# Kernel optimization log

Measured on AMD Instinct MI355X. Metric: run time of the kernel, lower is better.

Reference implementation:

```python
import jax, jax.numpy as jnp
import numpy as np
import math

D_KEY = 64
SCALE = math.sqrt(D_KEY)
INF = 1e10  # finite stand-in for the original INF constant
CAUSAL = True
DIAG = False


def setup_inputs() -> dict:
    key = jax.random.key(0)
    kq, kk, kv = jax.random.split(key, 3)
    B, L, D = 16, 2048, D_KEY
    return {
        "query": jax.random.normal(kq, (B, L, D), dtype=jnp.float32),
        "key": jax.random.normal(kk, (B, L, D), dtype=jnp.float32),
        "value": jax.random.normal(kv, (B, L, D), dtype=jnp.float32),
    }


def reference(query, key, value):
    # scores: [B, Lq, Lk]
    scores = jnp.einsum("bqd,bkd->bqk", query, key)
    L = key.shape[1]
    if CAUSAL:
        # subtract INF above the diagonal (strict upper triangle), as in torch triu(1)
        tri = jnp.triu(jnp.full((L, L), INF, dtype=scores.dtype), k=1)
        scores = scores - tri[None, :, :]
    if DIAG:
        # original scatters -INF onto the diagonal along dim 1
        diag_mask = jnp.eye(L, dtype=bool)
        scores = jnp.where(diag_mask[None, :, :], -INF, scores)
    # softmax over keys after scaling; dropout with p=0.0 is identity
    attn = jax.nn.softmax(scores / SCALE, axis=-1)
    return jnp.einsum("bqk,bkd->bqd", attn, value)
```

## Files before the change

kernel.cpp:

```cpp
#include <hip/hip_runtime.h>

typedef __bf16 bf16_t;
typedef __bf16 bf16x4 __attribute__((ext_vector_type(4)));
typedef __bf16 bf16x8 __attribute__((ext_vector_type(8)));
typedef float  f32x4  __attribute__((ext_vector_type(4)));

#define B_SZ  16
#define L_SEQ 2048
#define D_H   64
#define QB    64
#define KB    128
#define NQT   (L_SEQ / QB)

#define QSCALE 0.18033688011112043f

__global__ __launch_bounds__(256, 2)
void attn_fwd_kernel(const float* __restrict__ Qg, const float* __restrict__ Kg,
                     const float* __restrict__ Vg, float* __restrict__ Og)
{
    const int lin  = blockIdx.x;
    const int xcd  = lin & 7;
    const int slot = lin >> 3;
    const int half = slot >> 5;
    const int qi   = slot & 31;
    const int b    = xcd * 2 + half;
    const int qt   = half ? qi : (31 - qi);

    const int tid  = threadIdx.x;
    const int lane = tid & 63;
    const int lg   = lane >> 4;
    const int lc   = lane & 15;

    __shared__ __align__(16) bf16_t K_lds[2][KB][72];
    __shared__ __align__(16) bf16_t Vt_lds[2][D_H][136];

    const size_t bbase = (size_t)b * L_SEQ * D_H;

    const int qrow = qt * QB + (tid >> 6) * 16 + lc;
    bf16x8 qa[2];
#pragma unroll
    for (int h = 0; h < 2; ++h) {
        const float* qp = Qg + bbase + (size_t)qrow * D_H + h * 32 + lg * 8;
        const f32x4 f0 = *reinterpret_cast<const f32x4*>(qp);
        const f32x4 f1 = *reinterpret_cast<const f32x4*>(qp + 4);
        bf16x8 a;
#pragma unroll
        for (int j = 0; j < 4; ++j) { a[j] = (bf16_t)(f0[j] * QSCALE); a[4 + j] = (bf16_t)(f1[j] * QSCALE); }
        qa[h] = a;
    }

    f32x4 o[4];
#pragma unroll
    for (int dt = 0; dt < 4; ++dt) o[dt] = (f32x4){0.f, 0.f, 0.f, 0.f};
    float m = -1e30f, l = 0.f;

    const int nkt = (qt + 2) >> 1;

    const int vkb = tid & 31;
    const int vdg = tid >> 5;
    const int vpos = ((vkb >> 3) << 5) + ((vkb & 3) << 3) + (((vkb >> 2) & 1) << 2);

    f32x4 kreg[8], vreg[8];

    auto issueK = [&](int kt) {
        const int kbase = kt * KB;
#pragma unroll
        for (int i = 0; i < 8; ++i) {
            const int f = i * 256 + tid;
            const int r = f >> 4, c4 = (f & 15) * 4;
            kreg[i] = *reinterpret_cast<const f32x4*>(Kg + bbase + (size_t)(kbase + r) * D_H + c4);
        }
    };
    auto issueV = [&](int kt) {
        const int kbase = kt * KB;
#pragma unroll
        for (int d2 = 0; d2 < 2; ++d2)
#pragma unroll
            for (int i = 0; i < 4; ++i)
                vreg[d2 * 4 + i] = *reinterpret_cast<const f32x4*>(
                    Vg + bbase + (size_t)(kbase + vkb * 4 + i) * D_H + (vdg + d2 * 8) * 4);
    };
    auto writeK = [&](int buf) {
#pragma unroll
        for (int i = 0; i < 8; ++i) {
            const int f = i * 256 + tid;
            const int r = f >> 4, c4 = (f & 15) * 4;
            bf16x4 k4 = { (bf16_t)kreg[i][0], (bf16_t)kreg[i][1], (bf16_t)kreg[i][2], (bf16_t)kreg[i][3] };
            *reinterpret_cast<bf16x4*>(&K_lds[buf][r][c4]) = k4;
        }
    };
    auto writeV = [&](int buf) {
#pragma unroll
        for (int d2 = 0; d2 < 2; ++d2) {
            const int db = vdg + d2 * 8;
#pragma unroll
            for (int j = 0; j < 4; ++j) {
                bf16x4 cj = { (bf16_t)vreg[d2 * 4 + 0][j], (bf16_t)vreg[d2 * 4 + 1][j],
                              (bf16_t)vreg[d2 * 4 + 2][j], (bf16_t)vreg[d2 * 4 + 3][j] };
                *reinterpret_cast<bf16x4*>(&Vt_lds[buf][db * 4 + j][vpos]) = cj;
            }
        }
    };

    issueK(0); issueV(0); writeK(0); writeV(0);
    __syncthreads();
    int cur = 0;
    for (int kt = 0; kt < nkt; ++kt) {
        const bool last = (kt == nkt - 1);
        const int kbase = kt * KB;
        if (!last) issueK(kt + 1);

        f32x4 s[8];
        __builtin_amdgcn_s_setprio(1);
#pragma unroll
        for (int n = 0; n < 8; ++n) {
            f32x4 acc = (f32x4){0.f, 0.f, 0.f, 0.f};
#pragma unroll
            for (int h = 0; h < 2; ++h) {
                const bf16x8 kb = *reinterpret_cast<const bf16x8*>(&K_lds[cur][n * 16 + lc][h * 32 + lg * 8]);
                acc = __builtin_amdgcn_mfma_f32_16x16x32_bf16(kb, qa[h], acc, 0, 0, 0);
            }
            s[n] = acc;
        }
        __builtin_amdgcn_s_setprio(0);
        if (!last) issueV(kt + 1);
        if (last) {
#pragma unroll
            for (int n = 0; n < 8; ++n)
#pragma unroll
                for (int r = 0; r < 4; ++r)
                    if (kbase + n * 16 + lg * 4 + r > qrow) s[n][r] = -1e30f;
        }

        float mx = -1e30f;
#pragma unroll
        for (int n = 0; n < 8; ++n) {
            mx = fmaxf(fmaxf(mx, s[n][0]), fmaxf(s[n][1], fmaxf(s[n][2], s[n][3])));
        }
        mx = fmaxf(mx, __shfl_xor(mx, 16));
        mx = fmaxf(mx, __shfl_xor(mx, 32));
        const float mn = fmaxf(m, mx);
        const float alpha = exp2f(m - mn);
        m = mn;
        bf16x8 w[4];
        float rs = 0.f;
#pragma unroll
        for (int n = 0; n < 8; ++n) {
            const float p0 = exp2f(s[n][0] - mn), p1 = exp2f(s[n][1] - mn);
            const float p2 = exp2f(s[n][2] - mn), p3 = exp2f(s[n][3] - mn);
            rs += (p0 + p1) + (p2 + p3);
            const int wi = n >> 1, off = (n & 1) * 4;
            w[wi][off + 0] = (bf16_t)p0; w[wi][off + 1] = (bf16_t)p1;
            w[wi][off + 2] = (bf16_t)p2; w[wi][off + 3] = (bf16_t)p3;
        }
        rs += __shfl_xor(rs, 16);
        rs += __shfl_xor(rs, 32);
        l = l * alpha + rs;
#pragma unroll
        for (int dt = 0; dt < 4; ++dt)
#pragma unroll
            for (int r = 0; r < 4; ++r) o[dt][r] *= alpha;

        if (!last) writeK(cur ^ 1);

        __builtin_amdgcn_s_setprio(1);
#pragma unroll
        for (int ks = 0; ks < 4; ++ks) {
#pragma unroll
            for (int dt = 0; dt < 4; ++dt) {
                const bf16x8 vb = *reinterpret_cast<const bf16x8*>(&Vt_lds[cur][dt * 16 + lc][ks * 32 + lg * 8]);
                o[dt] = __builtin_amdgcn_mfma_f32_16x16x32_bf16(vb, w[ks], o[dt], 0, 0, 0);
            }
        }
        __builtin_amdgcn_s_setprio(0);

        if (!last) writeV(cur ^ 1);
        __syncthreads();
        cur ^= 1;
    }

    const float inv = 1.0f / l;
#pragma unroll
    for (int dt = 0; dt < 4; ++dt) {
        f32x4 val = { o[dt][0] * inv, o[dt][1] * inv, o[dt][2] * inv, o[dt][3] * inv };
        *reinterpret_cast<f32x4*>(Og + bbase + (size_t)qrow * D_H + dt * 16 + lg * 4) = val;
    }
}

extern "C" void kernel_launch(void* const* d_in, const int* in_sizes, int n_in,
                              void* d_out, int out_size, void* d_ws, size_t ws_size,
                              hipStream_t stream)
{
    const float* Q = (const float*)d_in[0];
    const float* K = (const float*)d_in[1];
    const float* V = (const float*)d_in[2];
    float* O = (float*)d_out;
    attn_fwd_kernel<<<dim3(NQT * B_SZ), dim3(256), 0, stream>>>(Q, K, V, O);
}
```

Before: 39.70 us.

## Split KV range across two wave groups and pair complementary causal q-tiles per block

Blocks grow to 512 threads, organised as two 256-thread groups. The groups process alternating KV tiles for the same query tile, and their partial softmax states (m, l, O) are merged through LDS at the end. Each block handles a pair of complementary query tiles (qt and 31-qt) in sequence, which balances causal work per block, and the grid shrinks to 256 blocks. This aims to improve load balance and per-tile parallelism. In exchange it doubles LDS use, adds merge synchronisation, and leaves fewer blocks to hide latency.

```diff
diff --git a/kernel.cpp b/kernel.cpp
--- a/kernel.cpp
+++ b/kernel.cpp
@@ -10,54 +10,33 @@
 #define D_H   64
 #define QB    64
 #define KB    128
-#define NQT   (L_SEQ / QB)
 
 #define QSCALE 0.18033688011112043f
 
-__global__ __launch_bounds__(256, 2)
+__global__ __launch_bounds__(512, 2)
 void attn_fwd_kernel(const float* __restrict__ Qg, const float* __restrict__ Kg,
                      const float* __restrict__ Vg, float* __restrict__ Og)
 {
-    const int lin  = blockIdx.x;
-    const int xcd  = lin & 7;
-    const int slot = lin >> 3;
-    const int half = slot >> 5;
-    const int qi   = slot & 31;
-    const int b    = xcd * 2 + half;
-    const int qt   = half ? qi : (31 - qi);
+    const int lin = blockIdx.x;
+    const int xcd = lin & 7;
+    const int b   = xcd * 2 + ((lin >> 3) & 1);
+    const int pi  = lin >> 4;
 
     const int tid  = threadIdx.x;
+    const int grp  = tid >> 8;
+    const int t8   = tid & 255;
+    const int wig  = t8 >> 6;
     const int lane = tid & 63;
     const int lg   = lane >> 4;
     const int lc   = lane & 15;
 
-    __shared__ __align__(16) bf16_t K_lds[2][KB][72];
-    __shared__ __align__(16) bf16_t Vt_lds[2][D_H][136];
+    __shared__ __align__(16) bf16_t K_lds[2][2][KB][72];
+    __shared__ __align__(16) bf16_t Vt_lds[2][2][D_H][136];
 
     const size_t bbase = (size_t)b * L_SEQ * D_H;
 
-    const int qrow = qt * QB + (tid >> 6) * 16 + lc;
-    bf16x8 qa[2];
-#pragma unroll
-    for (int h = 0; h < 2; ++h) {
-        const float* qp = Qg + bbase + (size_t)qrow * D_H + h * 32 + lg * 8;
-        const f32x4 f0 = *reinterpret_cast<const f32x4*>(qp);
-        const f32x4 f1 = *reinterpret_cast<const f32x4*>(qp + 4);
-        bf16x8 a;
-#pragma unroll
-        for (int j = 0; j < 4; ++j) { a[j] = (bf16_t)(f0[j] * QSCALE); a[4 + j] = (bf16_t)(f1[j] * QSCALE); }
-        qa[h] = a;
-    }
-
-    f32x4 o[4];
-#pragma unroll
-    for (int dt = 0; dt < 4; ++dt) o[dt] = (f32x4){0.f, 0.f, 0.f, 0.f};
-    float m = -1e30f, l = 0.f;
-
-    const int nkt = (qt + 2) >> 1;
-
-    const int vkb = tid & 31;
-    const int vdg = tid >> 5;
+    const int vkb  = t8 & 31;
+    const int vdg  = t8 >> 5;
     const int vpos = ((vkb >> 3) << 5) + ((vkb & 3) << 3) + (((vkb >> 2) & 1) << 2);
 
     f32x4 kreg[8], vreg[8];
@@ -66,7 +45,7 @@
         const int kbase = kt * KB;
 #pragma unroll
         for (int i = 0; i < 8; ++i) {
-            const int f = i * 256 + tid;
+            const int f = i * 256 + t8;
             const int r = f >> 4, c4 = (f & 15) * 4;
             kreg[i] = *reinterpret_cast<const f32x4*>(Kg + bbase + (size_t)(kbase + r) * D_H + c4);
         }
@@ -83,10 +62,10 @@
     auto writeK = [&](int buf) {
 #pragma unroll
         for (int i = 0; i < 8; ++i) {
-            const int f = i * 256 + tid;
+            const int f = i * 256 + t8;
             const int r = f >> 4, c4 = (f & 15) * 4;
             bf16x4 k4 = { (bf16_t)kreg[i][0], (bf16_t)kreg[i][1], (bf16_t)kreg[i][2], (bf16_t)kreg[i][3] };
-            *reinterpret_cast<bf16x4*>(&K_lds[buf][r][c4]) = k4;
+            *reinterpret_cast<bf16x4*>(&K_lds[grp][buf][r][c4]) = k4;
         }
     };
     auto writeV = [&](int buf) {
@@ -97,93 +76,142 @@
             for (int j = 0; j < 4; ++j) {
                 bf16x4 cj = { (bf16_t)vreg[d2 * 4 + 0][j], (bf16_t)vreg[d2 * 4 + 1][j],
                               (bf16_t)vreg[d2 * 4 + 2][j], (bf16_t)vreg[d2 * 4 + 3][j] };
-                *reinterpret_cast<bf16x4*>(&Vt_lds[buf][db * 4 + j][vpos]) = cj;
+                *reinterpret_cast<bf16x4*>(&Vt_lds[grp][buf][db * 4 + j][vpos]) = cj;
             }
         }
     };
 
-    issueK(0); issueV(0); writeK(0); writeV(0);
-    __syncthreads();
-    int cur = 0;
-    for (int kt = 0; kt < nkt; ++kt) {
-        const bool last = (kt == nkt - 1);
-        const int kbase = kt * KB;
-        if (!last) issueK(kt + 1);
-
-        f32x4 s[8];
-        __builtin_amdgcn_s_setprio(1);
-#pragma unroll
-        for (int n = 0; n < 8; ++n) {
-            f32x4 acc = (f32x4){0.f, 0.f, 0.f, 0.f};
-#pragma unroll
-            for (int h = 0; h < 2; ++h) {
-                const bf16x8 kb = *reinterpret_cast<const bf16x8*>(&K_lds[cur][n * 16 + lc][h * 32 + lg * 8]);
-                acc = __builtin_amdgcn_mfma_f32_16x16x32_bf16(kb, qa[h], acc, 0, 0, 0);
+    for (int hv = 0; hv < 2; ++hv) {
+        const int qt  = hv ? pi : (31 - pi);
+        const int nkt = (qt + 2) >> 1;
+        const int nsG = (nkt + 1 - grp) >> 1;
+        const int ns0 = (nkt + 1) >> 1;
+
+        const int qrow = qt * QB + wig * 16 + lc;
+        bf16x8 qa[2];
+#pragma unroll
+        for (int h = 0; h < 2; ++h) {
+            const float* qp = Qg + bbase + (size_t)qrow * D_H + h * 32 + lg * 8;
+            const f32x4 f0 = *reinterpret_cast<const f32x4*>(qp);
+            const f32x4 f1 = *reinterpret_cast<const f32x4*>(qp + 4);
+            bf16x8 a;
+#pragma unroll
+            for (int j = 0; j < 4; ++j) { a[j] = (bf16_t)(f0[j] * QSCALE); a[4 + j] = (bf16_t)(f1[j] * QSCALE); }
+            qa[h] = a;
+        }
+
+        f32x4 o[4];
+#pragma unroll
+        for (int dt = 0; dt < 4; ++dt) o[dt] = (f32x4){0.f, 0.f, 0.f, 0.f};
+        float m = -1e30f, l = 0.f;
+
+        if (nsG > 0) { issueK(grp); issueV(grp); writeK(0); writeV(0); }
+        __syncthreads();
+
+        int cur = 0;
+        for (int s = 0; s < ns0; ++s) {
+            if (s < nsG) {
+                const int kt    = 2 * s + grp;
+                const int kbase = kt * KB;
+                const bool more = (s + 1 < nsG);
+                if (more) issueK(2 * (s + 1) + grp);
+
+                f32x4 sc[8];
+                __builtin_amdgcn_s_setprio(1);
+#pragma unroll
+                for (int n = 0; n < 8; ++n) {
+                    f32x4 acc = (f32x4){0.f, 0.f, 0.f, 0.f};
+#pragma unroll
+                    for (int h = 0; h < 2; ++h) {
+                        const bf16x8 kb = *reinterpret_cast<const bf16x8*>(&K_lds[grp][cur][n * 16 + lc][h * 32 + lg * 8]);
+                        acc = __builtin_amdgcn_mfma_f32_16x16x32_bf16(kb, qa[h], acc, 0, 0, 0);
+                    }
+                    sc[n] = acc;
+                }
+                __builtin_amdgcn_s_setprio(0);
+                if (more) issueV(2 * (s + 1) + grp);
+                if (kt == nkt - 1) {
+#pragma unroll
+                    for (int n = 0; n < 8; ++n)
+#pragma unroll
+                        for (int r = 0; r < 4; ++r)
+                            if (kbase + n * 16 + lg * 4 + r > qrow) sc[n][r] = -1e30f;
+                }
+
+                float mx = -1e30f;
+#pragma unroll
+                for (int n = 0; n < 8; ++n)
+                    mx = fmaxf(fmaxf(mx, sc[n][0]), fmaxf(sc[n][1], fmaxf(sc[n][2], sc[n][3])));
+                mx = fmaxf(mx, __shfl_xor(mx, 16));
+                mx = fmaxf(mx, __shfl_xor(mx, 32));
+                const float mn = fmaxf(m, mx);
+                const float alpha = exp2f(m - mn);
+                m = mn;
+                bf16x8 w[4];
+                float rs = 0.f;
+#pragma unroll
+                for (int n = 0; n < 8; ++n) {
+                    const float p0 = exp2f(sc[n][0] - mn), p1 = exp2f(sc[n][1] - mn);
+                    const float p2 = exp2f(sc[n][2] - mn), p3 = exp2f(sc[n][3] - mn);
+                    rs += (p0 + p1) + (p2 + p3);
+                    const int wi = n >> 1, off = (n & 1) * 4;
+                    w[wi][off + 0] = (bf16_t)p0; w[wi][off + 1] = (bf16_t)p1;
+                    w[wi][off + 2] = (bf16_t)p2; w[wi][off + 3] = (bf16_t)p3;
+                }
+                rs += __shfl_xor(rs, 16);
+                rs += __shfl_xor(rs, 32);
+                l = l * alpha + rs;
+#pragma unroll
+                for (int dt = 0; dt < 4; ++dt)
+#pragma unroll
+                    for (int r = 0; r < 4; ++r) o[dt][r] *= alpha;
+
+                if (more) writeK(cur ^ 1);
+
+                __builtin_amdgcn_s_setprio(1);
+#pragma unroll
+                for (int ks = 0; ks < 4; ++ks) {
+#pragma unroll
+                    for (int dt = 0; dt < 4; ++dt) {
+                        const bf16x8 vb = *reinterpret_cast<const bf16x8*>(&Vt_lds[grp][cur][dt * 16 + lc][ks * 32 + lg * 8]);
+                        o[dt] = __builtin_amdgcn_mfma_f32_16x16x32_bf16(vb, w[ks], o[dt], 0, 0, 0);
+                    }
+                }
+                __builtin_amdgcn_s_setprio(0);
+
+                if (more) writeV(cur ^ 1);
             }
-            s[n] = acc;
-        }
-        __builtin_amdgcn_s_setprio(0);
-        if (!last) issueV(kt + 1);
-        if (last) {
-#pragma unroll
-            for (int n = 0; n < 8; ++n)
-#pragma unroll
-                for (int r = 0; r < 4; ++r)
-                    if (kbase + n * 16 + lg * 4 + r > qrow) s[n][r] = -1e30f;
-        }
-
-        float mx = -1e30f;
-#pragma unroll
-        for (int n = 0; n < 8; ++n) {
-            mx = fmaxf(fmaxf(mx, s[n][0]), fmaxf(s[n][1], fmaxf(s[n][2], s[n][3])));
-        }
-        mx = fmaxf(mx, __shfl_xor(mx, 16));
-        mx = fmaxf(mx, __shfl_xor(mx, 32));
-        const float mn = fmaxf(m, mx);
-        const float alpha = exp2f(m - mn);
-        m = mn;
-        bf16x8 w[4];
-        float rs = 0.f;
-#pragma unroll
-        for (int n = 0; n < 8; ++n) {
-            const float p0 = exp2f(s[n][0] - mn), p1 = exp2f(s[n][1] - mn);
-            const float p2 = exp2f(s[n][2] - mn), p3 = exp2f(s[n][3] - mn);
-            rs += (p0 + p1) + (p2 + p3);
-            const int wi = n >> 1, off = (n & 1) * 4;
-            w[wi][off + 0] = (bf16_t)p0; w[wi][off + 1] = (bf16_t)p1;
-            w[wi][off + 2] = (bf16_t)p2; w[wi][off + 3] = (bf16_t)p3;
-        }
-        rs += __shfl_xor(rs, 16);
-        rs += __shfl_xor(rs, 32);
-        l = l * alpha + rs;
-#pragma unroll
-        for (int dt = 0; dt < 4; ++dt)
-#pragma unroll
-            for (int r = 0; r < 4; ++r) o[dt][r] *= alpha;
-
-        if (!last) writeK(cur ^ 1);
-
-        __builtin_amdgcn_s_setprio(1);
-#pragma unroll
-        for (int ks = 0; ks < 4; ++ks) {
+            __syncthreads();
+            cur ^= 1;
+        }
+
+        float* mrg  = reinterpret_cast<float*>(&K_lds[0][0][0][0]);
+        float* obuf = mrg;
+        float* mbuf = mrg + 64 * 68;
+        float* lbuf = mrg + 64 * 68 + 64;
+        const int qq = wig * 16 + lc;
+        if (grp == 1) {
+#pragma unroll
+            for (int dt = 0; dt < 4; ++dt)
+                *reinterpret_cast<f32x4*>(&obuf[qq * 68 + dt * 16 + lg * 4]) = o[dt];
+            if (lg == 0) { mbuf[qq] = m; lbuf[qq] = l; }
+        }
+        __syncthreads();
+        if (grp == 0) {
+            const float m1 = mbuf[qq], l1 = lbuf[qq];
+            const float mt = fmaxf(m, m1);
+            const float a0 = exp2f(m - mt), a1 = exp2f(m1 - mt);
+            const float linv = 1.0f / (l * a0 + l1 * a1);
 #pragma unroll
             for (int dt = 0; dt < 4; ++dt) {
-                const bf16x8 vb = *reinterpret_cast<const bf16x8*>(&Vt_lds[cur][dt * 16 + lc][ks * 32 + lg * 8]);
-                o[dt] = __builtin_amdgcn_mfma_f32_16x16x32_bf16(vb, w[ks], o[dt], 0, 0, 0);
+                const f32x4 o1 = *reinterpret_cast<const f32x4*>(&obuf[qq * 68 + dt * 16 + lg * 4]);
+                f32x4 val;
+#pragma unroll
+                for (int r = 0; r < 4; ++r) val[r] = (o[dt][r] * a0 + o1[r] * a1) * linv;
+                *reinterpret_cast<f32x4*>(Og + bbase + (size_t)qrow * D_H + dt * 16 + lg * 4) = val;
             }
         }
-        __builtin_amdgcn_s_setprio(0);
-
-        if (!last) writeV(cur ^ 1);
         __syncthreads();
-        cur ^= 1;
-    }
-
-    const float inv = 1.0f / l;
-#pragma unroll
-    for (int dt = 0; dt < 4; ++dt) {
-        f32x4 val = { o[dt][0] * inv, o[dt][1] * inv, o[dt][2] * inv, o[dt][3] * inv };
-        *reinterpret_cast<f32x4*>(Og + bbase + (size_t)qrow * D_H + dt * 16 + lg * 4) = val;
     }
 }
 
@@ -195,5 +223,5 @@
     const float* K = (const float*)d_in[1];
     const float* V = (const float*)d_in[2];
     float* O = (float*)d_out;
-    attn_fwd_kernel<<<dim3(NQT * B_SZ), dim3(256), 0, stream>>>(Q, K, V, O);
+    attn_fwd_kernel<<<dim3(256), dim3(512), 0, stream>>>(Q, K, V, O);
 }
```

New measurement: 40.36 us. Within noise of the previous version (+1.7%).

## Swizzle K/V shared-memory layout, lazily rescale softmax, defer row-sum reduction

Applied to the files above, without the earlier changes.

Replaces the padded K and transposed-V LDS arrays with unpadded XOR-swizzled layouts and widens the K global loads and LDS writes to 8-element chunks. The online softmax now rescales the running max, sum and output only when some lane's new maximum exceeds the old one by more than a threshold of 8 (log2 domain), which skips the exp and multiply work in most iterations. The per-lane row sum is reduced across lanes once at the end instead of every tile. The target is fewer LDS bank conflicts, fewer LDS write instructions and less softmax and shuffle work per tile, at the cost of more index arithmetic and a bound on exponent growth before rescaling.

```diff
diff --git a/kernel.cpp b/kernel.cpp
--- a/kernel.cpp
+++ b/kernel.cpp
@@ -10,7 +10,6 @@
 #define D_H   64
 #define QB    64
 #define KB    128
-#define NQT   (L_SEQ / QB)
 
 #define QSCALE 0.18033688011112043f
 
@@ -30,9 +29,10 @@
     const int lane = tid & 63;
     const int lg   = lane >> 4;
     const int lc   = lane & 15;
-
-    __shared__ __align__(16) bf16_t K_lds[2][KB][72];
-    __shared__ __align__(16) bf16_t Vt_lds[2][D_H][136];
+    const int lc7  = lc & 7;
+
+    __shared__ __align__(16) bf16_t K_lds[2][KB * D_H];
+    __shared__ __align__(16) bf16_t Vt_lds[2][D_H * KB];
 
     const size_t bbase = (size_t)b * L_SEQ * D_H;
 
@@ -56,8 +56,8 @@
 
     const int nkt = (qt + 2) >> 1;
 
-    const int vkb = tid & 31;
-    const int vdg = tid >> 5;
+    const int vkb  = tid & 31;
+    const int vdg  = tid >> 5;
     const int vpos = ((vkb >> 3) << 5) + ((vkb & 3) << 3) + (((vkb >> 2) & 1) << 2);
 
     f32x4 kreg[8], vreg[8];
@@ -65,10 +65,12 @@
     auto issueK = [&](int kt) {
         const int kbase = kt * KB;
 #pragma unroll
-        for (int i = 0; i < 8; ++i) {
-            const int f = i * 256 + tid;
-            const int r = f >> 4, c4 = (f & 15) * 4;
-            kreg[i] = *reinterpret_cast<const f32x4*>(Kg + bbase + (size_t)(kbase + r) * D_H + c4);
+        for (int i = 0; i < 4; ++i) {
+            const int u = i * 256 + tid;
+            const int r = u >> 3, ch = u & 7;
+            const float* p = Kg + bbase + (size_t)(kbase + r) * D_H + ch * 8;
+            kreg[2 * i]     = *reinterpret_cast<const f32x4*>(p);
+            kreg[2 * i + 1] = *reinterpret_cast<const f32x4*>(p + 4);
         }
     };
     auto issueV = [&](int kt) {
@@ -82,11 +84,13 @@
     };
     auto writeK = [&](int buf) {
 #pragma unroll
-        for (int i = 0; i < 8; ++i) {
-            const int f = i * 256 + tid;
-            const int r = f >> 4, c4 = (f & 15) * 4;
-            bf16x4 k4 = { (bf16_t)kreg[i][0], (bf16_t)kreg[i][1], (bf16_t)kreg[i][2], (bf16_t)kreg[i][3] };
-            *reinterpret_cast<bf16x4*>(&K_lds[buf][r][c4]) = k4;
+        for (int i = 0; i < 4; ++i) {
+            const int u = i * 256 + tid;
+            const int r = u >> 3, ch = u & 7;
+            bf16x8 kk;
+#pragma unroll
+            for (int j = 0; j < 4; ++j) { kk[j] = (bf16_t)kreg[2 * i][j]; kk[4 + j] = (bf16_t)kreg[2 * i + 1][j]; }
+            *reinterpret_cast<bf16x8*>(&K_lds[buf][r * 64 + ((ch ^ (r & 7)) << 3)]) = kk;
         }
     };
     auto writeV = [&](int buf) {
@@ -95,9 +99,11 @@
             const int db = vdg + d2 * 8;
 #pragma unroll
             for (int j = 0; j < 4; ++j) {
+                const int d = db * 4 + j;
                 bf16x4 cj = { (bf16_t)vreg[d2 * 4 + 0][j], (bf16_t)vreg[d2 * 4 + 1][j],
                               (bf16_t)vreg[d2 * 4 + 2][j], (bf16_t)vreg[d2 * 4 + 3][j] };
-                *reinterpret_cast<bf16x4*>(&Vt_lds[buf][db * 4 + j][vpos]) = cj;
+                const int hw = d * 128 + (((vpos >> 3) ^ (d & 7)) << 3) + (vpos & 7);
+                *reinterpret_cast<bf16x4*>(&Vt_lds[buf][hw]) = cj;
             }
         }
     };
@@ -110,17 +116,18 @@
         const int kbase = kt * KB;
         if (!last) issueK(kt + 1);
 
-        f32x4 s[8];
+        f32x4 sc[8];
         __builtin_amdgcn_s_setprio(1);
 #pragma unroll
         for (int n = 0; n < 8; ++n) {
             f32x4 acc = (f32x4){0.f, 0.f, 0.f, 0.f};
 #pragma unroll
             for (int h = 0; h < 2; ++h) {
-                const bf16x8 kb = *reinterpret_cast<const bf16x8*>(&K_lds[cur][n * 16 + lc][h * 32 + lg * 8]);
+                const int hw = (n * 16 + lc) * 64 + ((((h << 2) | lg) ^ lc7) << 3);
+                const bf16x8 kb = *reinterpret_cast<const bf16x8*>(&K_lds[cur][hw]);
                 acc = __builtin_amdgcn_mfma_f32_16x16x32_bf16(kb, qa[h], acc, 0, 0, 0);
             }
-            s[n] = acc;
+            sc[n] = acc;
         }
         __builtin_amdgcn_s_setprio(0);
         if (!last) issueV(kt + 1);
@@ -129,37 +136,38 @@
             for (int n = 0; n < 8; ++n)
 #pragma unroll
                 for (int r = 0; r < 4; ++r)
-                    if (kbase + n * 16 + lg * 4 + r > qrow) s[n][r] = -1e30f;
-        }
-
-        float mx = -1e30f;
-#pragma unroll
-        for (int n = 0; n < 8; ++n) {
-            mx = fmaxf(fmaxf(mx, s[n][0]), fmaxf(s[n][1], fmaxf(s[n][2], s[n][3])));
-        }
-        mx = fmaxf(mx, __shfl_xor(mx, 16));
-        mx = fmaxf(mx, __shfl_xor(mx, 32));
-        const float mn = fmaxf(m, mx);
-        const float alpha = exp2f(m - mn);
-        m = mn;
+                    if (kbase + n * 16 + lg * 4 + r > qrow) sc[n][r] = -1e30f;
+        }
+
+        float mxp = fmaxf(fmaxf(sc[0][0], sc[0][1]), fmaxf(sc[0][2], sc[0][3]));
+#pragma unroll
+        for (int n = 1; n < 8; ++n)
+            mxp = fmaxf(mxp, fmaxf(fmaxf(sc[n][0], sc[n][1]), fmaxf(sc[n][2], sc[n][3])));
+        if (!__all(mxp <= m + 8.0f)) {
+            float mx = mxp;
+            mx = fmaxf(mx, __shfl_xor(mx, 16));
+            mx = fmaxf(mx, __shfl_xor(mx, 32));
+            const float mn = fmaxf(m, mx);
+            const float alpha = exp2f(m - mn);
+            m = mn;
+            l *= alpha;
+#pragma unroll
+            for (int dt = 0; dt < 4; ++dt)
+#pragma unroll
+                for (int r = 0; r < 4; ++r) o[dt][r] *= alpha;
+        }
         bf16x8 w[4];
         float rs = 0.f;
 #pragma unroll
         for (int n = 0; n < 8; ++n) {
-            const float p0 = exp2f(s[n][0] - mn), p1 = exp2f(s[n][1] - mn);
-            const float p2 = exp2f(s[n][2] - mn), p3 = exp2f(s[n][3] - mn);
+            const float p0 = exp2f(sc[n][0] - m), p1 = exp2f(sc[n][1] - m);
+            const float p2 = exp2f(sc[n][2] - m), p3 = exp2f(sc[n][3] - m);
             rs += (p0 + p1) + (p2 + p3);
             const int wi = n >> 1, off = (n & 1) * 4;
             w[wi][off + 0] = (bf16_t)p0; w[wi][off + 1] = (bf16_t)p1;
             w[wi][off + 2] = (bf16_t)p2; w[wi][off + 3] = (bf16_t)p3;
         }
-        rs += __shfl_xor(rs, 16);
-        rs += __shfl_xor(rs, 32);
-        l = l * alpha + rs;
-#pragma unroll
-        for (int dt = 0; dt < 4; ++dt)
-#pragma unroll
-            for (int r = 0; r < 4; ++r) o[dt][r] *= alpha;
+        l += rs;
 
         if (!last) writeK(cur ^ 1);
 
@@ -168,7 +176,8 @@
         for (int ks = 0; ks < 4; ++ks) {
 #pragma unroll
             for (int dt = 0; dt < 4; ++dt) {
-                const bf16x8 vb = *reinterpret_cast<const bf16x8*>(&Vt_lds[cur][dt * 16 + lc][ks * 32 + lg * 8]);
+                const int hw = (dt * 16 + lc) * 128 + ((((ks << 2) | lg) ^ lc7) << 3);
+                const bf16x8 vb = *reinterpret_cast<const bf16x8*>(&Vt_lds[cur][hw]);
                 o[dt] = __builtin_amdgcn_mfma_f32_16x16x32_bf16(vb, w[ks], o[dt], 0, 0, 0);
             }
         }
@@ -179,7 +188,10 @@
         cur ^= 1;
     }
 
-    const float inv = 1.0f / l;
+    float lr = l;
+    lr += __shfl_xor(lr, 16);
+    lr += __shfl_xor(lr, 32);
+    const float inv = 1.0f / lr;
 #pragma unroll
     for (int dt = 0; dt < 4; ++dt) {
         f32x4 val = { o[dt][0] * inv, o[dt][1] * inv, o[dt][2] * inv, o[dt][3] * inv };
@@ -195,5 +207,5 @@
     const float* K = (const float*)d_in[1];
     const float* V = (const float*)d_in[2];
     float* O = (float*)d_out;
-    attn_fwd_kernel<<<dim3(NQT * B_SZ), dim3(256), 0, stream>>>(Q, K, V, O);
+    attn_fwd_kernel<<<dim3(512), dim3(256), 0, stream>>>(Q, K, V, O);
 }
```

New measurement: 40.14 us. Within noise of the previous version (+1.1%).

## Split block into producer loader waves and consumer MFMA waves with lazy rescale

Applied to the files above, without the earlier changes.

The block grows to 512 threads. Four waves only load K/V from global memory, convert them to bf16 and write the double-buffered LDS tiles, while the other four waves do the QK and PV MFMAs and the softmax, with the two groups synchronised by block barriers. The consumers also skip the running-max rescale when no lane's new max exceeds the old one by more than a threshold, and defer the cross-lane row-sum reduction to the end. This is meant to overlap global-load latency with compute and to cut softmax ALU and shuffle work. The cost is more threads per CU, possible LDS write/read races around the single barrier per iteration, and some numerical risk from the threshold-based lazy rescale.

```diff
diff --git a/kernel.cpp b/kernel.cpp
--- a/kernel.cpp
+++ b/kernel.cpp
@@ -14,9 +14,9 @@
 
 #define QSCALE 0.18033688011112043f
 
-__global__ __launch_bounds__(256, 2)
-void attn_fwd_kernel(const float* __restrict__ Qg, const float* __restrict__ Kg,
-                     const float* __restrict__ Vg, float* __restrict__ Og)
+__global__ __launch_bounds__(512, 4)
+void attn_pc_kernel(const float* __restrict__ Qg, const float* __restrict__ Kg,
+                    const float* __restrict__ Vg, float* __restrict__ Og)
 {
     const int lin  = blockIdx.x;
     const int xcd  = lin & 7;
@@ -27,6 +27,7 @@
     const int qt   = half ? qi : (31 - qi);
 
     const int tid  = threadIdx.x;
+    const int wave = tid >> 6;
     const int lane = tid & 63;
     const int lg   = lane >> 4;
     const int lc   = lane & 15;
@@ -35,155 +36,164 @@
     __shared__ __align__(16) bf16_t Vt_lds[2][D_H][136];
 
     const size_t bbase = (size_t)b * L_SEQ * D_H;
-
-    const int qrow = qt * QB + (tid >> 6) * 16 + lc;
-    bf16x8 qa[2];
-#pragma unroll
-    for (int h = 0; h < 2; ++h) {
-        const float* qp = Qg + bbase + (size_t)qrow * D_H + h * 32 + lg * 8;
-        const f32x4 f0 = *reinterpret_cast<const f32x4*>(qp);
-        const f32x4 f1 = *reinterpret_cast<const f32x4*>(qp + 4);
-        bf16x8 a;
-#pragma unroll
-        for (int j = 0; j < 4; ++j) { a[j] = (bf16_t)(f0[j] * QSCALE); a[4 + j] = (bf16_t)(f1[j] * QSCALE); }
-        qa[h] = a;
-    }
-
-    f32x4 o[4];
-#pragma unroll
-    for (int dt = 0; dt < 4; ++dt) o[dt] = (f32x4){0.f, 0.f, 0.f, 0.f};
-    float m = -1e30f, l = 0.f;
-
     const int nkt = (qt + 2) >> 1;
 
-    const int vkb = tid & 31;
-    const int vdg = tid >> 5;
-    const int vpos = ((vkb >> 3) << 5) + ((vkb & 3) << 3) + (((vkb >> 2) & 1) << 2);
-
-    f32x4 kreg[8], vreg[8];
-
-    auto issueK = [&](int kt) {
-        const int kbase = kt * KB;
-#pragma unroll
-        for (int i = 0; i < 8; ++i) {
-            const int f = i * 256 + tid;
-            const int r = f >> 4, c4 = (f & 15) * 4;
-            kreg[i] = *reinterpret_cast<const f32x4*>(Kg + bbase + (size_t)(kbase + r) * D_H + c4);
-        }
-    };
-    auto issueV = [&](int kt) {
-        const int kbase = kt * KB;
-#pragma unroll
-        for (int d2 = 0; d2 < 2; ++d2)
-#pragma unroll
-            for (int i = 0; i < 4; ++i)
-                vreg[d2 * 4 + i] = *reinterpret_cast<const f32x4*>(
-                    Vg + bbase + (size_t)(kbase + vkb * 4 + i) * D_H + (vdg + d2 * 8) * 4);
-    };
-    auto writeK = [&](int buf) {
-#pragma unroll
-        for (int i = 0; i < 8; ++i) {
-            const int f = i * 256 + tid;
-            const int r = f >> 4, c4 = (f & 15) * 4;
-            bf16x4 k4 = { (bf16_t)kreg[i][0], (bf16_t)kreg[i][1], (bf16_t)kreg[i][2], (bf16_t)kreg[i][3] };
-            *reinterpret_cast<bf16x4*>(&K_lds[buf][r][c4]) = k4;
-        }
-    };
-    auto writeV = [&](int buf) {
-#pragma unroll
-        for (int d2 = 0; d2 < 2; ++d2) {
-            const int db = vdg + d2 * 8;
-#pragma unroll
-            for (int j = 0; j < 4; ++j) {
-                bf16x4 cj = { (bf16_t)vreg[d2 * 4 + 0][j], (bf16_t)vreg[d2 * 4 + 1][j],
-                              (bf16_t)vreg[d2 * 4 + 2][j], (bf16_t)vreg[d2 * 4 + 3][j] };
-                *reinterpret_cast<bf16x4*>(&Vt_lds[buf][db * 4 + j][vpos]) = cj;
-            }
-        }
-    };
-
-    issueK(0); issueV(0); writeK(0); writeV(0);
-    __syncthreads();
-    int cur = 0;
-    for (int kt = 0; kt < nkt; ++kt) {
-        const bool last = (kt == nkt - 1);
-        const int kbase = kt * KB;
-        if (!last) issueK(kt + 1);
-
-        f32x4 s[8];
-        __builtin_amdgcn_s_setprio(1);
-#pragma unroll
-        for (int n = 0; n < 8; ++n) {
-            f32x4 acc = (f32x4){0.f, 0.f, 0.f, 0.f};
-#pragma unroll
-            for (int h = 0; h < 2; ++h) {
-                const bf16x8 kb = *reinterpret_cast<const bf16x8*>(&K_lds[cur][n * 16 + lc][h * 32 + lg * 8]);
-                acc = __builtin_amdgcn_mfma_f32_16x16x32_bf16(kb, qa[h], acc, 0, 0, 0);
-            }
-            s[n] = acc;
-        }
-        __builtin_amdgcn_s_setprio(0);
-        if (!last) issueV(kt + 1);
-        if (last) {
-#pragma unroll
-            for (int n = 0; n < 8; ++n)
-#pragma unroll
-                for (int r = 0; r < 4; ++r)
-                    if (kbase + n * 16 + lg * 4 + r > qrow) s[n][r] = -1e30f;
-        }
-
-        float mx = -1e30f;
-#pragma unroll
-        for (int n = 0; n < 8; ++n) {
-            mx = fmaxf(fmaxf(mx, s[n][0]), fmaxf(s[n][1], fmaxf(s[n][2], s[n][3])));
-        }
-        mx = fmaxf(mx, __shfl_xor(mx, 16));
-        mx = fmaxf(mx, __shfl_xor(mx, 32));
-        const float mn = fmaxf(m, mx);
-        const float alpha = exp2f(m - mn);
-        m = mn;
-        bf16x8 w[4];
-        float rs = 0.f;
-#pragma unroll
-        for (int n = 0; n < 8; ++n) {
-            const float p0 = exp2f(s[n][0] - mn), p1 = exp2f(s[n][1] - mn);
-            const float p2 = exp2f(s[n][2] - mn), p3 = exp2f(s[n][3] - mn);
-            rs += (p0 + p1) + (p2 + p3);
-            const int wi = n >> 1, off = (n & 1) * 4;
-            w[wi][off + 0] = (bf16_t)p0; w[wi][off + 1] = (bf16_t)p1;
-            w[wi][off + 2] = (bf16_t)p2; w[wi][off + 3] = (bf16_t)p3;
-        }
-        rs += __shfl_xor(rs, 16);
-        rs += __shfl_xor(rs, 32);
-        l = l * alpha + rs;
-#pragma unroll
-        for (int dt = 0; dt < 4; ++dt)
-#pragma unroll
-            for (int r = 0; r < 4; ++r) o[dt][r] *= alpha;
-
-        if (!last) writeK(cur ^ 1);
-
-        __builtin_amdgcn_s_setprio(1);
-#pragma unroll
-        for (int ks = 0; ks < 4; ++ks) {
-#pragma unroll
-            for (int dt = 0; dt < 4; ++dt) {
-                const bf16x8 vb = *reinterpret_cast<const bf16x8*>(&Vt_lds[cur][dt * 16 + lc][ks * 32 + lg * 8]);
-                o[dt] = __builtin_amdgcn_mfma_f32_16x16x32_bf16(vb, w[ks], o[dt], 0, 0, 0);
-            }
-        }
-        __builtin_amdgcn_s_setprio(0);
-
-        if (!last) writeV(cur ^ 1);
+    if (wave >= 4) {
+        const int pt   = tid - 256;
+        const int vkb  = pt & 31;
+        const int vdg  = pt >> 5;
+        const int vpos = ((vkb >> 3) << 5) + ((vkb & 3) << 3) + (((vkb >> 2) & 1) << 2);
+
+        f32x4 kreg[8], vreg[8];
+
+        auto issueK = [&](int kt) {
+            const int kbase = kt * KB;
+#pragma unroll
+            for (int i = 0; i < 8; ++i) {
+                const int f = i * 256 + pt;
+                const int r = f >> 4, c4 = (f & 15) * 4;
+                kreg[i] = *reinterpret_cast<const f32x4*>(Kg + bbase + (size_t)(kbase + r) * D_H + c4);
+            }
+        };
+        auto issueV = [&](int kt) {
+            const int kbase = kt * KB;
+#pragma unroll
+            for (int d2 = 0; d2 < 2; ++d2)
+#pragma unroll
+                for (int i = 0; i < 4; ++i)
+                    vreg[d2 * 4 + i] = *reinterpret_cast<const f32x4*>(
+                        Vg + bbase + (size_t)(kbase + vkb * 4 + i) * D_H + (vdg + d2 * 8) * 4);
+        };
+        auto writeK = [&](int buf) {
+#pragma unroll
+            for (int i = 0; i < 8; ++i) {
+                const int f = i * 256 + pt;
+                const int r = f >> 4, c4 = (f & 15) * 4;
+                bf16x4 k4 = { (bf16_t)kreg[i][0], (bf16_t)kreg[i][1], (bf16_t)kreg[i][2], (bf16_t)kreg[i][3] };
+                *reinterpret_cast<bf16x4*>(&K_lds[buf][r][c4]) = k4;
+            }
+        };
+        auto writeV = [&](int buf) {
+#pragma unroll
+            for (int d2 = 0; d2 < 2; ++d2) {
+                const int db = vdg + d2 * 8;
+#pragma unroll
+                for (int j = 0; j < 4; ++j) {
+                    bf16x4 cj = { (bf16_t)vreg[d2 * 4 + 0][j], (bf16_t)vreg[d2 * 4 + 1][j],
+                                  (bf16_t)vreg[d2 * 4 + 2][j], (bf16_t)vreg[d2 * 4 + 3][j] };
+                    *reinterpret_cast<bf16x4*>(&Vt_lds[buf][db * 4 + j][vpos]) = cj;
+                }
+            }
+        };
+
+        issueK(0); issueV(0); writeK(0); writeV(0);
         __syncthreads();
-        cur ^= 1;
-    }
-
-    const float inv = 1.0f / l;
-#pragma unroll
-    for (int dt = 0; dt < 4; ++dt) {
-        f32x4 val = { o[dt][0] * inv, o[dt][1] * inv, o[dt][2] * inv, o[dt][3] * inv };
-        *reinterpret_cast<f32x4*>(Og + bbase + (size_t)qrow * D_H + dt * 16 + lg * 4) = val;
+        for (int kt = 0; kt < nkt; ++kt) {
+            if (kt + 1 < nkt) {
+                issueK(kt + 1); issueV(kt + 1);
+                writeK((kt + 1) & 1); writeV((kt + 1) & 1);
+            }
+            __syncthreads();
+        }
+    } else {
+        const int qrow = qt * QB + wave * 16 + lc;
+        bf16x8 qa[2];
+#pragma unroll
+        for (int h = 0; h < 2; ++h) {
+            const float* qp = Qg + bbase + (size_t)qrow * D_H + h * 32 + lg * 8;
+            const f32x4 f0 = *reinterpret_cast<const f32x4*>(qp);
+            const f32x4 f1 = *reinterpret_cast<const f32x4*>(qp + 4);
+            bf16x8 a;
+#pragma unroll
+            for (int j = 0; j < 4; ++j) { a[j] = (bf16_t)(f0[j] * QSCALE); a[4 + j] = (bf16_t)(f1[j] * QSCALE); }
+            qa[h] = a;
+        }
+
+        f32x4 o[4];
+#pragma unroll
+        for (int dt = 0; dt < 4; ++dt) o[dt] = (f32x4){0.f, 0.f, 0.f, 0.f};
+        float m = -1e30f, l = 0.f;
+
+        __syncthreads();
+        for (int kt = 0; kt < nkt; ++kt) {
+            const bool last = (kt == nkt - 1);
+            const int kbase = kt * KB;
+            const int cur   = kt & 1;
+
+            f32x4 sc[8];
+            __builtin_amdgcn_s_setprio(1);
+#pragma unroll
+            for (int n = 0; n < 8; ++n) {
+                f32x4 acc = (f32x4){0.f, 0.f, 0.f, 0.f};
+#pragma unroll
+                for (int h = 0; h < 2; ++h) {
+                    const bf16x8 kb = *reinterpret_cast<const bf16x8*>(&K_lds[cur][n * 16 + lc][h * 32 + lg * 8]);
+                    acc = __builtin_amdgcn_mfma_f32_16x16x32_bf16(kb, qa[h], acc, 0, 0, 0);
+                }
+                sc[n] = acc;
+            }
+            __builtin_amdgcn_s_setprio(0);
+            if (last) {
+#pragma unroll
+                for (int n = 0; n < 8; ++n)
+#pragma unroll
+                    for (int r = 0; r < 4; ++r)
+                        if (kbase + n * 16 + lg * 4 + r > qrow) sc[n][r] = -1e30f;
+            }
+
+            float mxp = fmaxf(fmaxf(sc[0][0], sc[0][1]), fmaxf(sc[0][2], sc[0][3]));
+#pragma unroll
+            for (int n = 1; n < 8; ++n)
+                mxp = fmaxf(mxp, fmaxf(fmaxf(sc[n][0], sc[n][1]), fmaxf(sc[n][2], sc[n][3])));
+            if (!__all(mxp <= m + 8.0f)) {
+                float mx = mxp;
+                mx = fmaxf(mx, __shfl_xor(mx, 16));
+                mx = fmaxf(mx, __shfl_xor(mx, 32));
+                const float mn = fmaxf(m, mx);
+                const float alpha = exp2f(m - mn);
+                m = mn;
+                l *= alpha;
+#pragma unroll
+                for (int dt = 0; dt < 4; ++dt)
+#pragma unroll
+                    for (int r = 0; r < 4; ++r) o[dt][r] *= alpha;
+            }
+            bf16x8 w[4];
+            float rs = 0.f;
+#pragma unroll
+            for (int n = 0; n < 8; ++n) {
+                const float p0 = exp2f(sc[n][0] - m), p1 = exp2f(sc[n][1] - m);
+                const float p2 = exp2f(sc[n][2] - m), p3 = exp2f(sc[n][3] - m);
+                rs += (p0 + p1) + (p2 + p3);
+                const int wi = n >> 1, off = (n & 1) * 4;
+                w[wi][off + 0] = (bf16_t)p0; w[wi][off + 1] = (bf16_t)p1;
+                w[wi][off + 2] = (bf16_t)p2; w[wi][off + 3] = (bf16_t)p3;
+            }
+            l += rs;
+
+            __builtin_amdgcn_s_setprio(1);
+#pragma unroll
+            for (int ks = 0; ks < 4; ++ks) {
+#pragma unroll
+                for (int dt = 0; dt < 4; ++dt) {
+                    const bf16x8 vb = *reinterpret_cast<const bf16x8*>(&Vt_lds[cur][dt * 16 + lc][ks * 32 + lg * 8]);
+                    o[dt] = __builtin_amdgcn_mfma_f32_16x16x32_bf16(vb, w[ks], o[dt], 0, 0, 0);
+                }
+            }
+            __builtin_amdgcn_s_setprio(0);
+
+            __syncthreads();
+        }
+
+        float lr = l;
+        lr += __shfl_xor(lr, 16);
+        lr += __shfl_xor(lr, 32);
+        const float inv = 1.0f / lr;
+#pragma unroll
+        for (int dt = 0; dt < 4; ++dt) {
+            f32x4 val = { o[dt][0] * inv, o[dt][1] * inv, o[dt][2] * inv, o[dt][3] * inv };
+            *reinterpret_cast<f32x4*>(Og + bbase + (size_t)qrow * D_H + dt * 16 + lg * 4) = val;
+        }
     }
 }
 
@@ -195,5 +205,5 @@
     const float* K = (const float*)d_in[1];
     const float* V = (const float*)d_in[2];
     float* O = (float*)d_out;
-    attn_fwd_kernel<<<dim3(NQT * B_SZ), dim3(256), 0, stream>>>(Q, K, V, O);
+    attn_pc_kernel<<<dim3(NQT * B_SZ), dim3(512), 0, stream>>>(Q, K, V, O);
 }
```

After: 33.92 us (median of 3 runs). 1.17x faster.
